# Kernel optimization log

Measured on AMD Instinct MI355X. Metric: run time of the kernel, lower is better.

Reference implementation:

```python
import jax, jax.numpy as jnp
import numpy as np
from jax import lax

B, D, F, H = 1024, 64, 8, 256   # batch, state_dim, forcing_dim, hidden_dim
T, TU = 50, 128                  # eval points, forcing samples
N_SUB = 4                        # fixed dopri5 substeps per eval interval


def setup_inputs() -> dict:
    key = jax.random.key(0)
    k1, k2, k3, k4 = jax.random.split(key, 4)
    x0 = jax.random.normal(k1, (B, D), jnp.float32)
    t_eval = jnp.linspace(0.0, 1.0, T, dtype=jnp.float32)
    t_u = jnp.linspace(0.0, 1.0, TU, dtype=jnp.float32)
    u_batch = jax.random.normal(k2, (B, TU, F), jnp.float32)
    W1 = jax.random.normal(k3, (D + F, H), jnp.float32) / np.sqrt(D + F)
    b1 = jnp.zeros((H,), jnp.float32)
    W2 = jax.random.normal(k4, (H, D), jnp.float32) / np.sqrt(H)
    b2 = jnp.zeros((D,), jnp.float32)
    return {"x0": x0, "t_eval": t_eval, "t_u": t_u, "u_batch": u_batch,
            "W1": W1, "b1": b1, "W2": W2, "b2": b2}


def _interp_u(t, t_u, u_batch):
    # piecewise-linear forcing interpolation at scalar time t -> (B, F)
    idx = jnp.clip(jnp.searchsorted(t_u, t, side='right') - 1, 0, t_u.shape[0] - 2)
    t0, t1 = t_u[idx], t_u[idx + 1]
    w = (t - t0) / (t1 - t0)
    u0 = u_batch[:, idx, :]
    u1 = u_batch[:, idx + 1, :]
    return u0 + w * (u1 - u0)


def _odeint_dopri5(f, x0, t_eval):
    # Dormand-Prince RK45 (5th-order solution) with fixed substeps per interval.
    dt_coarse = jnp.diff(t_eval)                                   # [T-1]
    frac = jnp.arange(N_SUB, dtype=x0.dtype) / N_SUB               # [N_SUB]
    ts = (t_eval[:-1, None] + dt_coarse[:, None] * frac).reshape(-1)
    dts = jnp.repeat(dt_coarse / N_SUB, N_SUB)                     # [(T-1)*N_SUB]

    def step(x, tdt):
        t, dt = tdt
        k1 = f(t, x)
        k2 = f(t + dt / 5, x + dt * (k1 / 5))
        k3 = f(t + 3 * dt / 10, x + dt * (3 / 40 * k1 + 9 / 40 * k2))
        k4 = f(t + 4 * dt / 5, x + dt * (44 / 45 * k1 - 56 / 15 * k2 + 32 / 9 * k3))
        k5 = f(t + 8 * dt / 9, x + dt * (19372 / 6561 * k1 - 25360 / 2187 * k2
                                         + 64448 / 6561 * k3 - 212 / 729 * k4))
        k6 = f(t + dt, x + dt * (9017 / 3168 * k1 - 355 / 33 * k2 + 46732 / 5247 * k3
                                 + 49 / 176 * k4 - 5103 / 18656 * k5))
        x_new = x + dt * (35 / 384 * k1 + 500 / 1113 * k3 + 125 / 192 * k4
                          - 2187 / 6784 * k5 + 11 / 84 * k6)
        return x_new, x_new

    _, xs = lax.scan(step, x0, (ts, dts))          # [(T-1)*N_SUB, B, D]
    xs_eval = xs[N_SUB - 1::N_SUB]                  # states at t_eval[1:]
    return jnp.concatenate([x0[None], xs_eval], axis=0)  # [T, B, D]


def reference(x0, t_eval, t_u, u_batch, W1, b1, W2, b2):
    def ode_func(t, x):
        u = _interp_u(t, t_u, u_batch)              # (B, F)
        z = jnp.concatenate([x, u], axis=-1)        # (B, D+F)
        return jnp.tanh(z @ W1 + b1) @ W2 + b2      # (B, D)

    x_tb = _odeint_dopri5(ode_func, x0, t_eval)     # [T, B, D]
    return jnp.transpose(x_tb, (1, 0, 2))           # [B, T, D]
```

## Files before the change

kernel.cpp:

```cpp
#include <hip/hip_runtime.h>


typedef _Float16 half8 __attribute__((ext_vector_type(8)));
typedef float f32x4 __attribute__((ext_vector_type(4)));

#define MFMA16(a, b, c) __builtin_amdgcn_mfma_f32_16x16x32_f16((a), (b), (c), 0, 0, 0)

__global__ __launch_bounds__(256, 2)
void node_kernel(const float* __restrict__ x0,
                 const float* __restrict__ t_eval,
                 const float* __restrict__ t_u,
                 const float* __restrict__ u_batch,
                 const float* __restrict__ W1,
                 const float* __restrict__ b1,
                 const float* __restrict__ W2,
                 const float* __restrict__ b2,
                 float* __restrict__ out)
{
    __shared__ __align__(16) _Float16 zAh[8 * 144];
    __shared__ __align__(16) _Float16 hAh[32 * 144];
    __shared__ __align__(16) float ush[6][2][8];

    const int tid = threadIdx.x;
    const int wv  = tid >> 6;
    const int l   = tid & 63;
    const int lm  = l & 15;
    const int lq  = l >> 4;
    const int blk = blockIdx.x;

    const float C2L = 2.8853900817779268f;

    for (int i = tid; i < (8 * 144) / 2; i += 256)  ((uint32_t*)zAh)[i] = 0u;
    for (int i = tid; i < (32 * 144) / 2; i += 256) ((uint32_t*)hAh)[i] = 0u;

    half8 b1h[4][2];
    float b1b[4];
#pragma unroll
    for (int t = 0; t < 4; ++t) {
        const int n1 = (wv * 4 + t) * 16 + lm;
        b1b[t] = b1[n1] * C2L;
#pragma unroll
        for (int c = 0; c < 2; ++c) {
#pragma unroll
            for (int j = 0; j < 8; ++j) {
                const int k = c * 32 + lq * 8 + j;
                b1h[t][c][j] = (_Float16)(W1[k * 256 + n1] * C2L);
            }
        }
    }
    const int n1u = wv * 64 + l;
    float w1u[8];
#pragma unroll
    for (int f = 0; f < 8; ++f)
        w1u[f] = W1[(64 + f) * 256 + n1u] * C2L;

    const int n2 = wv * 16 + lm;
    half8 b2h[8];
#pragma unroll
    for (int cc = 0; cc < 8; ++cc) {
#pragma unroll
        for (int j = 0; j < 8; ++j) {
            const int k = cc * 32 + lq * 8 + j;
            b2h[cc][j] = (_Float16)W2[k * 64 + n2];
        }
    }
    const float b2b = b2[n2];

    float xr[2];
    float kfr[5][2];
#pragma unroll
    for (int r = 0; r < 2; ++r) {
        const int gr = blk * 2 + r;
        xr[r] = x0[gr * 64 + n2];
        if (lq == 0) out[gr * 3200 + n2] = xr[r];
    }
    __syncthreads();

#pragma unroll 1
    for (int step = 0; step < 196; ++step) {
        const int n = step >> 2;
        const int m = step & 3;
        const float te0 = t_eval[n];
        const float dtc = t_eval[n + 1] - te0;
        const float t   = te0 + dtc * (0.25f * (float)m);
        const float dt  = dtc * 0.25f;

        if (tid < 96) {
            const int s   = tid >> 4;
            const int rem = tid & 15;
            const int mr  = rem >> 3, f = rem & 7;
            float cs;
            switch (s) {
                case 0: cs = 0.0f; break;
                case 1: cs = 1.0f / 5.0f; break;
                case 2: cs = 3.0f / 10.0f; break;
                case 3: cs = 4.0f / 5.0f; break;
                case 4: cs = 8.0f / 9.0f; break;
                default: cs = 1.0f; break;
            }
            const float tsv = t + dt * cs;
            int iu = (int)(tsv * 127.0f);
            iu = iu < 0 ? 0 : (iu > 126 ? 126 : iu);
            const float ta = t_u[iu];
            const float tb = t_u[iu + 1];
            const float wt = (tsv - ta) / (tb - ta);
            const float* ub = &u_batch[(blk * 2 + mr) * 1024 + iu * 8 + f];
            const float u0v = ub[0];
            const float u1v = ub[8];
            ush[s][mr][f] = fmaf(wt, u1v - u0v, u0v);
        }
        __syncthreads();

#pragma unroll
        for (int s = 0; s < 6; ++s) {
            float zv[2];
#pragma unroll
            for (int r = 0; r < 2; ++r) {
                float v;
                if (s == 0)      v = xr[r];
                else if (s == 1) v = fmaf(dt, kfr[0][r] * (1.0f/5.0f), xr[r]);
                else if (s == 2) v = fmaf(dt, fmaf(3.0f/40.0f, kfr[0][r], (9.0f/40.0f)*kfr[1][r]), xr[r]);
                else if (s == 3) v = fmaf(dt, (44.0f/45.0f)*kfr[0][r] + (-56.0f/15.0f)*kfr[1][r]
                                             + (32.0f/9.0f)*kfr[2][r], xr[r]);
                else if (s == 4) v = fmaf(dt, (19372.0f/6561.0f)*kfr[0][r] + (-25360.0f/2187.0f)*kfr[1][r]
                                             + (64448.0f/6561.0f)*kfr[2][r] + (-212.0f/729.0f)*kfr[3][r], xr[r]);
                else             v = fmaf(dt, (9017.0f/3168.0f)*kfr[0][r] + (-355.0f/33.0f)*kfr[1][r]
                                             + (46732.0f/5247.0f)*kfr[2][r] + (49.0f/176.0f)*kfr[3][r]
                                             + (-5103.0f/18656.0f)*kfr[4][r], xr[r]);
                zv[r] = v;
            }
            if (lq == 0) {
#pragma unroll
                for (int r = 0; r < 2; ++r)
                    zAh[(n2 >> 3) * 144 + r * 8 + (n2 & 7)] = (_Float16)zv[r];
            }
            __syncthreads();

            const float4 uA0 = *(const float4*)&ush[s][0][0];
            const float4 uB0 = *(const float4*)&ush[s][0][4];
            const float4 uA1 = *(const float4*)&ush[s][1][0];
            const float4 uB1 = *(const float4*)&ush[s][1][4];
            float yu0 = uA0.x * w1u[0];
            yu0 = fmaf(uA0.y, w1u[1], yu0);
            yu0 = fmaf(uA0.z, w1u[2], yu0);
            yu0 = fmaf(uA0.w, w1u[3], yu0);
            yu0 = fmaf(uB0.x, w1u[4], yu0);
            yu0 = fmaf(uB0.y, w1u[5], yu0);
            yu0 = fmaf(uB0.z, w1u[6], yu0);
            yu0 = fmaf(uB0.w, w1u[7], yu0);
            float yu1 = uA1.x * w1u[0];
            yu1 = fmaf(uA1.y, w1u[1], yu1);
            yu1 = fmaf(uA1.z, w1u[2], yu1);
            yu1 = fmaf(uA1.w, w1u[3], yu1);
            yu1 = fmaf(uB1.x, w1u[4], yu1);
            yu1 = fmaf(uB1.y, w1u[5], yu1);
            yu1 = fmaf(uB1.z, w1u[6], yu1);
            yu1 = fmaf(uB1.w, w1u[7], yu1);

            half8 az[2];
#pragma unroll
            for (int c = 0; c < 2; ++c)
                az[c] = *(const half8*)&zAh[(c * 4 + lq) * 144 + lm * 8];
#pragma unroll
            for (int t = 0; t < 4; ++t) {
                f32x4 aHH = {0.f, 0.f, 0.f, 0.f};
                aHH = MFMA16(az[0], b1h[t][0], aHH);
                aHH = MFMA16(az[1], b1h[t][1], aHH);
                const float yut0 = __shfl(yu0, t * 16 + lm);
                const float yut1 = __shfl(yu1, t * 16 + lm);
                const int kqb = (wv * 4 + t) * 2 + (lm >> 3);
                const float y0 = aHH[0] + yut0 + b1b[t];
                const float y1 = aHH[1] + yut1 + b1b[t];
                const float e0 = __builtin_amdgcn_exp2f(y0);
                const float e1 = __builtin_amdgcn_exp2f(y1);
                const float h0 = fmaf(-2.0f, __builtin_amdgcn_rcpf(e0 + 1.0f), 1.0f);
                const float h1 = fmaf(-2.0f, __builtin_amdgcn_rcpf(e1 + 1.0f), 1.0f);
                if (lq == 0) {
                    hAh[kqb * 144 + (lm & 7)]     = (_Float16)h0;
                    hAh[kqb * 144 + 8 + (lm & 7)] = (_Float16)h1;
                }
            }
            __syncthreads();

            f32x4 aP = {0.f, 0.f, 0.f, 0.f};
            f32x4 aR = {0.f, 0.f, 0.f, 0.f};
#pragma unroll
            for (int cc = 0; cc < 8; cc += 2) {
                const half8 ah0 = *(const half8*)&hAh[((cc    ) * 4 + lq) * 144 + lm * 8];
                const half8 ah1 = *(const half8*)&hAh[((cc + 1) * 4 + lq) * 144 + lm * 8];
                aP = MFMA16(ah0, b2h[cc    ], aP);
                aR = MFMA16(ah1, b2h[cc + 1], aR);
            }
            if (s < 5) {
#pragma unroll
                for (int r = 0; r < 2; ++r)
                    kfr[s][r] = (aP[r] + aR[r]) + b2b;
            } else {
#pragma unroll
                for (int r = 0; r < 2; ++r) {
                    const float k6 = (aP[r] + aR[r]) + b2b;
                    xr[r] = fmaf(dt, (35.0f/384.0f)*kfr[0][r] + (500.0f/1113.0f)*kfr[2][r]
                                    + (125.0f/192.0f)*kfr[3][r] + (-2187.0f/6784.0f)*kfr[4][r]
                                    + (11.0f/84.0f)*k6, xr[r]);
                }
            }
        }

        if (m == 3 && lq == 0) {
#pragma unroll
            for (int r = 0; r < 2; ++r)
                out[(blk * 2 + r) * 3200 + (n + 1) * 64 + n2] = xr[r];
        }
    }
}

extern "C" void kernel_launch(void* const* d_in, const int* in_sizes, int n_in,
                              void* d_out, int out_size, void* d_ws, size_t ws_size,
                              hipStream_t stream) {
    const float* x0      = (const float*)d_in[0];
    const float* t_eval  = (const float*)d_in[1];
    const float* t_u     = (const float*)d_in[2];
    const float* u_batch = (const float*)d_in[3];
    const float* W1      = (const float*)d_in[4];
    const float* b1      = (const float*)d_in[5];
    const float* W2      = (const float*)d_in[6];
    const float* b2      = (const float*)d_in[7];
    float* out = (float*)d_out;

    node_kernel<<<dim3(512), dim3(256), 0, stream>>>(
        x0, t_eval, t_u, u_batch, W1, b1, W2, b2, out);
}
```

Baseline: 1.160 ms.

## Split block into specialized layer-1 and layer-2 waves with merged barriers

Doubles the block to 512 threads, with waves 0-3 holding W2 and doing the second GEMM plus the RK stage update, and waves 4-7 holding W1 and doing the first GEMM and tanh. The layer-2 GEMM is moved to the start of the next stage so it fuses with the z update, cutting per-stage barriers from three to two. It also shrinks the shared-memory padding and passes the forcing projection through shared memory instead of shuffles. Each wave now keeps only half the weight fragments in registers, but half the waves sit idle at every barrier, and the final k6 is handled in an epilogue.

Measured after the change: 1.262 ms. +8.8%, slower.

```diff
diff --git a/kernel.cpp b/kernel.cpp
--- a/kernel.cpp
+++ b/kernel.cpp
@@ -6,7 +6,7 @@
 
 #define MFMA16(a, b, c) __builtin_amdgcn_mfma_f32_16x16x32_f16((a), (b), (c), 0, 0, 0)
 
-__global__ __launch_bounds__(256, 2)
+__global__ __launch_bounds__(512, 1)
 void node_kernel(const float* __restrict__ x0,
                  const float* __restrict__ t_eval,
                  const float* __restrict__ t_u,
@@ -17,9 +17,10 @@
                  const float* __restrict__ b2,
                  float* __restrict__ out)
 {
-    __shared__ __align__(16) _Float16 zAh[8 * 144];
-    __shared__ __align__(16) _Float16 hAh[32 * 144];
-    __shared__ __align__(16) float ush[6][2][8];
+    __shared__ __align__(16) _Float16 zAh[8 * 24];
+    __shared__ __align__(16) _Float16 hAh[32 * 24];
+    __shared__ __align__(16) float    yus[256][2];
+    __shared__ __align__(16) float    ush[6][2][8];
 
     const int tid = threadIdx.x;
     const int wv  = tid >> 6;
@@ -30,51 +31,57 @@
 
     const float C2L = 2.8853900817779268f;
 
-    for (int i = tid; i < (8 * 144) / 2; i += 256)  ((uint32_t*)zAh)[i] = 0u;
-    for (int i = tid; i < (32 * 144) / 2; i += 256) ((uint32_t*)hAh)[i] = 0u;
-
-    half8 b1h[4][2];
-    float b1b[4];
-#pragma unroll
-    for (int t = 0; t < 4; ++t) {
-        const int n1 = (wv * 4 + t) * 16 + lm;
-        b1b[t] = b1[n1] * C2L;
-#pragma unroll
-        for (int c = 0; c < 2; ++c) {
-#pragma unroll
-            for (int j = 0; j < 8; ++j) {
-                const int k = c * 32 + lq * 8 + j;
-                b1h[t][c][j] = (_Float16)(W1[k * 256 + n1] * C2L);
-            }
-        }
-    }
-    const int n1u = wv * 64 + l;
+    for (int i = tid; i < (8 * 24) / 2; i += 512)  ((uint32_t*)zAh)[i] = 0u;
+    for (int i = tid; i < (32 * 24) / 2; i += 512) ((uint32_t*)hAh)[i] = 0u;
+
+    const int rowoff = (lm < 2 ? lm : 2) * 16;
+    const char* zb = (const char*)zAh + lq * 48 + rowoff;
+    const char* hb = (const char*)hAh + lq * 48 + rowoff;
+
+    half8 Wf[8];
+    float b1b[4] = {0.f, 0.f, 0.f, 0.f};
     float w1u[8];
-#pragma unroll
-    for (int f = 0; f < 8; ++f)
-        w1u[f] = W1[(64 + f) * 256 + n1u] * C2L;
-
-    const int n2 = wv * 16 + lm;
-    half8 b2h[8];
-#pragma unroll
-    for (int cc = 0; cc < 8; ++cc) {
-#pragma unroll
-        for (int j = 0; j < 8; ++j) {
-            const int k = cc * 32 + lq * 8 + j;
-            b2h[cc][j] = (_Float16)W2[k * 64 + n2];
-        }
-    }
-    const float b2b = b2[n2];
-
+    float b2b = 0.0f;
     float xr[2];
     float kfr[5][2];
-#pragma unroll
-    for (int r = 0; r < 2; ++r) {
-        const int gr = blk * 2 + r;
-        xr[r] = x0[gr * 64 + n2];
-        if (lq == 0) out[gr * 3200 + n2] = xr[r];
+    const int n2 = (wv & 3) * 16 + lm;
+
+    if (wv >= 4) {
+        const int g = wv - 4;
+#pragma unroll
+        for (int t = 0; t < 4; ++t) {
+            const int n1 = (g * 4 + t) * 16 + lm;
+            b1b[t] = b1[n1] * C2L;
+#pragma unroll
+            for (int c = 0; c < 2; ++c)
+#pragma unroll
+                for (int j = 0; j < 8; ++j) {
+                    const int k = c * 32 + lq * 8 + j;
+                    Wf[t * 2 + c][j] = (_Float16)(W1[k * 256 + n1] * C2L);
+                }
+        }
+    } else {
+#pragma unroll
+        for (int cc = 0; cc < 8; ++cc)
+#pragma unroll
+            for (int j = 0; j < 8; ++j) {
+                const int k = cc * 32 + lq * 8 + j;
+                Wf[cc][j] = (_Float16)W2[k * 64 + n2];
+            }
+        b2b = b2[n2];
+        const int n1u = wv * 64 + l;
+#pragma unroll
+        for (int f = 0; f < 8; ++f)
+            w1u[f] = W1[(64 + f) * 256 + n1u] * C2L;
+#pragma unroll
+        for (int r = 0; r < 2; ++r) {
+            xr[r] = x0[(blk * 2 + r) * 64 + n2];
+            if (lq == 0) out[(blk * 2 + r) * 3200 + n2] = xr[r];
+        }
     }
     __syncthreads();
+
+    float dt_prev = 0.0f;
 
 #pragma unroll 1
     for (int step = 0; step < 196; ++step) {
@@ -113,103 +120,135 @@
 
 #pragma unroll
         for (int s = 0; s < 6; ++s) {
-            float zv[2];
-#pragma unroll
-            for (int r = 0; r < 2; ++r) {
-                float v;
-                if (s == 0)      v = xr[r];
-                else if (s == 1) v = fmaf(dt, kfr[0][r] * (1.0f/5.0f), xr[r]);
-                else if (s == 2) v = fmaf(dt, fmaf(3.0f/40.0f, kfr[0][r], (9.0f/40.0f)*kfr[1][r]), xr[r]);
-                else if (s == 3) v = fmaf(dt, (44.0f/45.0f)*kfr[0][r] + (-56.0f/15.0f)*kfr[1][r]
-                                             + (32.0f/9.0f)*kfr[2][r], xr[r]);
-                else if (s == 4) v = fmaf(dt, (19372.0f/6561.0f)*kfr[0][r] + (-25360.0f/2187.0f)*kfr[1][r]
-                                             + (64448.0f/6561.0f)*kfr[2][r] + (-212.0f/729.0f)*kfr[3][r], xr[r]);
-                else             v = fmaf(dt, (9017.0f/3168.0f)*kfr[0][r] + (-355.0f/33.0f)*kfr[1][r]
-                                             + (46732.0f/5247.0f)*kfr[2][r] + (49.0f/176.0f)*kfr[3][r]
-                                             + (-5103.0f/18656.0f)*kfr[4][r], xr[r]);
-                zv[r] = v;
-            }
-            if (lq == 0) {
-#pragma unroll
-                for (int r = 0; r < 2; ++r)
-                    zAh[(n2 >> 3) * 144 + r * 8 + (n2 & 7)] = (_Float16)zv[r];
+            if (wv < 4) {
+                float kv[2] = {0.f, 0.f};
+                if (step > 0 || s > 0) {
+                    f32x4 aP = {0.f, 0.f, 0.f, 0.f};
+                    f32x4 aR = {0.f, 0.f, 0.f, 0.f};
+#pragma unroll
+                    for (int cc = 0; cc < 8; cc += 2) {
+                        const half8 ah0 = *(const half8*)(hb + cc * 192);
+                        const half8 ah1 = *(const half8*)(hb + cc * 192 + 192);
+                        aP = MFMA16(ah0, Wf[cc], aP);
+                        aR = MFMA16(ah1, Wf[cc + 1], aR);
+                    }
+                    kv[0] = (aP[0] + aR[0]) + b2b;
+                    kv[1] = (aP[1] + aR[1]) + b2b;
+                }
+                float zv[2];
+#pragma unroll
+                for (int r = 0; r < 2; ++r) {
+                    if (s == 0) {
+                        if (step > 0)
+                            xr[r] = fmaf(dt_prev, (35.0f/384.0f)*kfr[0][r] + (500.0f/1113.0f)*kfr[2][r]
+                                            + (125.0f/192.0f)*kfr[3][r] + (-2187.0f/6784.0f)*kfr[4][r]
+                                            + (11.0f/84.0f)*kv[r], xr[r]);
+                        zv[r] = xr[r];
+                    } else if (s == 1) {
+                        kfr[0][r] = kv[r];
+                        zv[r] = fmaf(dt, kv[r] * (1.0f/5.0f), xr[r]);
+                    } else if (s == 2) {
+                        kfr[1][r] = kv[r];
+                        zv[r] = fmaf(dt, fmaf(3.0f/40.0f, kfr[0][r], (9.0f/40.0f)*kv[r]), xr[r]);
+                    } else if (s == 3) {
+                        kfr[2][r] = kv[r];
+                        zv[r] = fmaf(dt, (44.0f/45.0f)*kfr[0][r] + (-56.0f/15.0f)*kfr[1][r]
+                                        + (32.0f/9.0f)*kv[r], xr[r]);
+                    } else if (s == 4) {
+                        kfr[3][r] = kv[r];
+                        zv[r] = fmaf(dt, (19372.0f/6561.0f)*kfr[0][r] + (-25360.0f/2187.0f)*kfr[1][r]
+                                        + (64448.0f/6561.0f)*kfr[2][r] + (-212.0f/729.0f)*kv[r], xr[r]);
+                    } else {
+                        kfr[4][r] = kv[r];
+                        zv[r] = fmaf(dt, (9017.0f/3168.0f)*kfr[0][r] + (-355.0f/33.0f)*kfr[1][r]
+                                        + (46732.0f/5247.0f)*kfr[2][r] + (49.0f/176.0f)*kfr[3][r]
+                                        + (-5103.0f/18656.0f)*kv[r], xr[r]);
+                    }
+                }
+                if (s == 0 && step > 0 && ((step - 1) & 3) == 3 && lq == 0) {
+                    const int ti = ((step - 1) >> 2) + 1;
+#pragma unroll
+                    for (int r = 0; r < 2; ++r)
+                        out[(blk * 2 + r) * 3200 + ti * 64 + n2] = xr[r];
+                }
+                if (lq == 0) {
+#pragma unroll
+                    for (int r = 0; r < 2; ++r)
+                        zAh[(n2 >> 3) * 24 + r * 8 + (n2 & 7)] = (_Float16)zv[r];
+                }
+                const float4 uA0 = *(const float4*)&ush[s][0][0];
+                const float4 uB0 = *(const float4*)&ush[s][0][4];
+                const float4 uA1 = *(const float4*)&ush[s][1][0];
+                const float4 uB1 = *(const float4*)&ush[s][1][4];
+                float yu0 = uA0.x * w1u[0];
+                yu0 = fmaf(uA0.y, w1u[1], yu0);
+                yu0 = fmaf(uA0.z, w1u[2], yu0);
+                yu0 = fmaf(uA0.w, w1u[3], yu0);
+                yu0 = fmaf(uB0.x, w1u[4], yu0);
+                yu0 = fmaf(uB0.y, w1u[5], yu0);
+                yu0 = fmaf(uB0.z, w1u[6], yu0);
+                yu0 = fmaf(uB0.w, w1u[7], yu0);
+                float yu1 = uA1.x * w1u[0];
+                yu1 = fmaf(uA1.y, w1u[1], yu1);
+                yu1 = fmaf(uA1.z, w1u[2], yu1);
+                yu1 = fmaf(uA1.w, w1u[3], yu1);
+                yu1 = fmaf(uB1.x, w1u[4], yu1);
+                yu1 = fmaf(uB1.y, w1u[5], yu1);
+                yu1 = fmaf(uB1.z, w1u[6], yu1);
+                yu1 = fmaf(uB1.w, w1u[7], yu1);
+                const int n1u = wv * 64 + l;
+                float2 yw; yw.x = yu0; yw.y = yu1;
+                *(float2*)&yus[n1u][0] = yw;
             }
             __syncthreads();
 
-            const float4 uA0 = *(const float4*)&ush[s][0][0];
-            const float4 uB0 = *(const float4*)&ush[s][0][4];
-            const float4 uA1 = *(const float4*)&ush[s][1][0];
-            const float4 uB1 = *(const float4*)&ush[s][1][4];
-            float yu0 = uA0.x * w1u[0];
-            yu0 = fmaf(uA0.y, w1u[1], yu0);
-            yu0 = fmaf(uA0.z, w1u[2], yu0);
-            yu0 = fmaf(uA0.w, w1u[3], yu0);
-            yu0 = fmaf(uB0.x, w1u[4], yu0);
-            yu0 = fmaf(uB0.y, w1u[5], yu0);
-            yu0 = fmaf(uB0.z, w1u[6], yu0);
-            yu0 = fmaf(uB0.w, w1u[7], yu0);
-            float yu1 = uA1.x * w1u[0];
-            yu1 = fmaf(uA1.y, w1u[1], yu1);
-            yu1 = fmaf(uA1.z, w1u[2], yu1);
-            yu1 = fmaf(uA1.w, w1u[3], yu1);
-            yu1 = fmaf(uB1.x, w1u[4], yu1);
-            yu1 = fmaf(uB1.y, w1u[5], yu1);
-            yu1 = fmaf(uB1.z, w1u[6], yu1);
-            yu1 = fmaf(uB1.w, w1u[7], yu1);
-
-            half8 az[2];
-#pragma unroll
-            for (int c = 0; c < 2; ++c)
-                az[c] = *(const half8*)&zAh[(c * 4 + lq) * 144 + lm * 8];
-#pragma unroll
-            for (int t = 0; t < 4; ++t) {
-                f32x4 aHH = {0.f, 0.f, 0.f, 0.f};
-                aHH = MFMA16(az[0], b1h[t][0], aHH);
-                aHH = MFMA16(az[1], b1h[t][1], aHH);
-                const float yut0 = __shfl(yu0, t * 16 + lm);
-                const float yut1 = __shfl(yu1, t * 16 + lm);
-                const int kqb = (wv * 4 + t) * 2 + (lm >> 3);
-                const float y0 = aHH[0] + yut0 + b1b[t];
-                const float y1 = aHH[1] + yut1 + b1b[t];
-                const float e0 = __builtin_amdgcn_exp2f(y0);
-                const float e1 = __builtin_amdgcn_exp2f(y1);
-                const float h0 = fmaf(-2.0f, __builtin_amdgcn_rcpf(e0 + 1.0f), 1.0f);
-                const float h1 = fmaf(-2.0f, __builtin_amdgcn_rcpf(e1 + 1.0f), 1.0f);
-                if (lq == 0) {
-                    hAh[kqb * 144 + (lm & 7)]     = (_Float16)h0;
-                    hAh[kqb * 144 + 8 + (lm & 7)] = (_Float16)h1;
+            if (wv >= 4) {
+                const int g = wv - 4;
+                const half8 az0 = *(const half8*)(zb);
+                const half8 az1 = *(const half8*)(zb + 192);
+#pragma unroll
+                for (int tt = 0; tt < 4; ++tt) {
+                    f32x4 aHH = {0.f, 0.f, 0.f, 0.f};
+                    aHH = MFMA16(az0, Wf[tt * 2 + 0], aHH);
+                    aHH = MFMA16(az1, Wf[tt * 2 + 1], aHH);
+                    const int T = g * 4 + tt;
+                    const float2 yu2 = *(const float2*)&yus[T * 16 + lm][0];
+                    const float y0 = aHH[0] + yu2.x + b1b[tt];
+                    const float y1 = aHH[1] + yu2.y + b1b[tt];
+                    const float e0 = __builtin_amdgcn_exp2f(y0);
+                    const float e1 = __builtin_amdgcn_exp2f(y1);
+                    const float h0 = fmaf(-2.0f, __builtin_amdgcn_rcpf(e0 + 1.0f), 1.0f);
+                    const float h1 = fmaf(-2.0f, __builtin_amdgcn_rcpf(e1 + 1.0f), 1.0f);
+                    const int pl = T * 2 + (lm >> 3);
+                    if (lq == 0) {
+                        hAh[pl * 24 + (lm & 7)]     = (_Float16)h0;
+                        hAh[pl * 24 + 8 + (lm & 7)] = (_Float16)h1;
+                    }
                 }
             }
             __syncthreads();
-
-            f32x4 aP = {0.f, 0.f, 0.f, 0.f};
-            f32x4 aR = {0.f, 0.f, 0.f, 0.f};
-#pragma unroll
-            for (int cc = 0; cc < 8; cc += 2) {
-                const half8 ah0 = *(const half8*)&hAh[((cc    ) * 4 + lq) * 144 + lm * 8];
-                const half8 ah1 = *(const half8*)&hAh[((cc + 1) * 4 + lq) * 144 + lm * 8];
-                aP = MFMA16(ah0, b2h[cc    ], aP);
-                aR = MFMA16(ah1, b2h[cc + 1], aR);
-            }
-            if (s < 5) {
-#pragma unroll
-                for (int r = 0; r < 2; ++r)
-                    kfr[s][r] = (aP[r] + aR[r]) + b2b;
-            } else {
-#pragma unroll
-                for (int r = 0; r < 2; ++r) {
-                    const float k6 = (aP[r] + aR[r]) + b2b;
-                    xr[r] = fmaf(dt, (35.0f/384.0f)*kfr[0][r] + (500.0f/1113.0f)*kfr[2][r]
-                                    + (125.0f/192.0f)*kfr[3][r] + (-2187.0f/6784.0f)*kfr[4][r]
-                                    + (11.0f/84.0f)*k6, xr[r]);
-                }
-            }
-        }
-
-        if (m == 3 && lq == 0) {
-#pragma unroll
-            for (int r = 0; r < 2; ++r)
-                out[(blk * 2 + r) * 3200 + (n + 1) * 64 + n2] = xr[r];
+        }
+        dt_prev = dt;
+    }
+
+    if (wv < 4) {
+        f32x4 aP = {0.f, 0.f, 0.f, 0.f};
+        f32x4 aR = {0.f, 0.f, 0.f, 0.f};
+#pragma unroll
+        for (int cc = 0; cc < 8; cc += 2) {
+            const half8 ah0 = *(const half8*)(hb + cc * 192);
+            const half8 ah1 = *(const half8*)(hb + cc * 192 + 192);
+            aP = MFMA16(ah0, Wf[cc], aP);
+            aR = MFMA16(ah1, Wf[cc + 1], aR);
+        }
+#pragma unroll
+        for (int r = 0; r < 2; ++r) {
+            const float k6 = (aP[r] + aR[r]) + b2b;
+            xr[r] = fmaf(dt_prev, (35.0f/384.0f)*kfr[0][r] + (500.0f/1113.0f)*kfr[2][r]
+                            + (125.0f/192.0f)*kfr[3][r] + (-2187.0f/6784.0f)*kfr[4][r]
+                            + (11.0f/84.0f)*k6, xr[r]);
+            if (lq == 0)
+                out[(blk * 2 + r) * 3200 + 49 * 64 + n2] = xr[r];
         }
     }
 }
@@ -227,6 +266,6 @@
     const float* b2      = (const float*)d_in[7];
     float* out = (float*)d_out;
 
-    node_kernel<<<dim3(512), dim3(256), 0, stream>>>(
+    node_kernel<<<dim3(512), dim3(512), 0, stream>>>(
         x0, t_eval, t_u, u_batch, W1, b1, W2, b2, out);
 }
```
